# Kernel tuning notes

Measured on AMD Instinct MI355X. Metric: run time of the kernel, lower is better.

Reference implementation:

```python
import jax, jax.numpy as jnp
import numpy as np

BS, Q, S1, S2 = 8, 128, 32, 64
H_DIM, NH = 768, 12
DH = H_DIM // NH


def _linear_params(k, scale=0.02):
    kw, _ = jax.random.split(k)
    w = jax.random.normal(kw, (H_DIM, H_DIM), jnp.float32) * scale
    b = jnp.zeros((H_DIM,), jnp.float32)
    return w, b


def setup_inputs() -> dict:
    root = jax.random.key(0)
    ks = jax.random.split(root, 12)
    wq_w, wq_b = _linear_params(ks[0])
    wk_w, wk_b = _linear_params(ks[1])
    wv_w, wv_b = _linear_params(ks[2])
    sq_w, sq_b = _linear_params(ks[3])
    sk_w, sk_b = _linear_params(ks[4])
    sv_w, sv_b = _linear_params(ks[5])
    return {
        "q_in": jax.random.normal(ks[6], (BS, Q, H_DIM), jnp.float32),
        "k_in": jax.random.normal(ks[7], (BS, S1, S2, H_DIM), jnp.float32),
        "v_in": jax.random.normal(ks[8], (BS, S1, S2, H_DIM), jnp.float32),
        "kvec": jax.random.normal(ks[9], (BS, S1, H_DIM), jnp.float32),
        "word_mask": jnp.ones((BS, S1, S2), jnp.int32),
        "sentence_mask": jnp.ones((BS * Q, S1), jnp.int32),
        "wq_w": wq_w, "wq_b": wq_b, "wk_w": wk_w, "wk_b": wk_b,
        "wv_w": wv_w, "wv_b": wv_b, "sq_w": sq_w, "sq_b": sq_b,
        "sk_w": sk_w, "sk_b": sk_b, "sv_w": sv_w, "sv_b": sv_b,
    }


def reference(q_in, k_in, v_in, kvec, word_mask, sentence_mask,
              wq_w, wq_b, wk_w, wk_b, wv_w, wv_b,
              sq_w, sq_b, sk_w, sk_b, sv_w, sv_b):
    bs, q_len = q_in.shape[0], q_in.shape[1]
    s1, s2 = k_in.shape[1], k_in.shape[2]
    scale = 1.0 / jnp.sqrt(jnp.float32(DH))

    # additive masks, as in the torch module
    wm = (1.0 - word_mask.astype(jnp.float32)) * -10000.0      # [bs, s1, s2]
    sm = (1.0 - sentence_mask.astype(jnp.float32)) * -10000.0  # [bs*Q, s1]

    # ---- word-level attention ----
    q = (q_in @ wq_w + wq_b).reshape(bs, q_len, NH, DH)
    k = (k_in @ wk_w + wk_b).reshape(bs, s1, s2, NH, DH)
    v = (v_in @ wv_w + wv_b).reshape(bs, s1, s2, NH, DH)
    # scores over tokens within each sentence: [bs, s1, H, Q, s2]
    scores1 = jnp.einsum('bqhd,bsthd->bshqt', q, k) * scale
    probs1 = jax.nn.softmax(scores1 + wm[:, :, None, None, :], axis=-1)
    # word_hidden: [bs, Q, s1, h]
    wh = jnp.einsum('bshqt,bsthd->bqshd', probs1, v).reshape(bs, q_len, s1, H_DIM)

    # ---- sentence-level attention ----
    sq = (q_in @ sq_w + sq_b).reshape(bs, q_len, NH, DH)
    sk = (kvec @ sk_w + sk_b).reshape(bs, s1, NH, DH)   # shared across queries
    sv = (wh @ sv_w + sv_b).reshape(bs, q_len, s1, NH, DH)
    scores2 = jnp.einsum('bqhd,bshd->bqhs', sq, sk) * scale  # [bs, Q, H, s1]
    scores2 = scores2 + sm.reshape(bs, q_len, s1)[:, :, None, :]
    probs2 = jax.nn.softmax(scores2, axis=-1)
    out = jnp.einsum('bqhs,bqshd->bqhd', probs2, sv).reshape(bs * q_len, H_DIM)
    return out
```

## Files before the change

### kernel.cpp

```cpp
#include <hip/hip_runtime.h>
#include <hip/hip_bf16.h>


typedef __attribute__((ext_vector_type(8))) short short8;
typedef __attribute__((ext_vector_type(4))) short short4v;
typedef __attribute__((ext_vector_type(4))) float f32x4;

__device__ __forceinline__ short f2bf(float f) {
  __hip_bfloat16 b = __float2bfloat16(f);
  return __builtin_bit_cast(short, b);
}
__device__ __forceinline__ float bf2f(short s) {
  __hip_bfloat16 b = __builtin_bit_cast(__hip_bfloat16, s);
  return __bfloat162float(b);
}

#define MFMA16(a, b, c) __builtin_amdgcn_mfma_f32_16x16x32_bf16((a), (b), (c), 0, 0, 0)

__device__ __forceinline__ void async_load16(const void* g, void* l) {
  auto l3 = (__attribute__((address_space(3))) void*)(uintptr_t)(
      reinterpret_cast<uintptr_t>(l));
  auto g1 = (const __attribute__((address_space(1))) void*)g;
  __builtin_amdgcn_global_load_lds(g1, l3, 16, 0, 0);
}

__global__ __launch_bounds__(256)
void prep(const float* __restrict__ w0, const float* __restrict__ w1,
          const float* __restrict__ w2, const float* __restrict__ w3,
          const float* __restrict__ w4, const float* __restrict__ w5,
          short* __restrict__ WT,
          const float* __restrict__ q_in, const float* __restrict__ k_in,
          const float* __restrict__ v_in, const float* __restrict__ kvec,
          short* __restrict__ qbf, short* __restrict__ kbf,
          short* __restrict__ vbf, short* __restrict__ kvb) {
  const int id = blockIdx.x;
  const int tid = threadIdx.x;
  if (id < 3456) {
    __shared__ float tile[32][33];
    const int zz = id / 576, r = id % 576;
    const float* W = (zz == 0) ? w0 : (zz == 1) ? w1 : (zz == 2) ? w2
                   : (zz == 3) ? w3 : (zz == 4) ? w4 : w5;
    short* WTo = WT + (size_t)zz * 768 * 768;
    const int bx = (r % 24) * 32, by = (r / 24) * 32;
    const int tx = tid & 31, ty = tid >> 5;
    #pragma unroll
    for (int i = 0; i < 32; i += 8)
      tile[ty + i][tx] = W[(size_t)(by + ty + i) * 768 + bx + tx];
    __syncthreads();
    #pragma unroll
    for (int i = 0; i < 32; i += 8)
      WTo[(size_t)(bx + ty + i) * 768 + by + tx] = f2bf(tile[tx][ty + i]);
    return;
  }
  const int i = (id - 3456) * 256 + tid;
  const float* src;
  short* dst;
  int idx;
  if (i < 98304)        { src = q_in; dst = qbf; idx = i; }
  else if (i < 1671168) { src = k_in; dst = kbf; idx = i - 98304; }
  else if (i < 3244032) { src = v_in; dst = vbf; idx = i - 1671168; }
  else                  { src = kvec; dst = kvb; idx = i - 3244032; }
  const float4* s = (const float4*)src + (size_t)idx * 2;
  const float4 a = s[0], b = s[1];
  __align__(16) short tmp[8] = {f2bf(a.x), f2bf(a.y), f2bf(a.z), f2bf(a.w),
                                f2bf(b.x), f2bf(b.y), f2bf(b.z), f2bf(b.w)};
  *((short8*)dst + idx) = *(short8*)tmp;
}

__global__ __launch_bounds__(256)
void gemm_proj(const short* __restrict__ kbf, const short* __restrict__ vbf,
               const short* __restrict__ qbf, const short* __restrict__ kvb,
               const short* __restrict__ WT6,
               const float* __restrict__ wk_b, const float* __restrict__ wv_b,
               const float* __restrict__ wq_b, const float* __restrict__ sq_b,
               const float* __restrict__ sk_b,
               short* __restrict__ kp, short* __restrict__ vT,
               short* __restrict__ qp, float* __restrict__ sqp,
               float* __restrict__ skp) {
  const int K = 768, WELEM = 768 * 768;
  __shared__ __align__(16) short As[128 * 64];
  __shared__ __align__(16) short Bs[128 * 64];
  const int tid = threadIdx.x;
  const int w = tid >> 6, lane = tid & 63, quad = lane >> 4, l16 = lane & 15;
  const int wm = (w >> 1) * 64, wn = (w & 1) * 64;
  const f32x4 zero4 = {0.f, 0.f, 0.f, 0.f};

  if (blockIdx.z < 2) {
    const int z = blockIdx.z;
    const short* A = z ? vbf : kbf;
    const short* WT = z ? (WT6 + 3 * WELEM) : (WT6 + 2 * WELEM);
    const float* bias = z ? wv_b : wk_b;
    const int m0 = blockIdx.x * 128, n0 = blockIdx.y * 128;

    const int srow = lane >> 3;
    const int ssw = (lane & 7) ^ srow;
    const short* ag = A + (size_t)(m0 + w * 32 + srow) * K + ssw * 8;
    const short* bg = WT + (size_t)(n0 + w * 32 + srow) * K + ssw * 8;
    short* al = &As[(w * 32) * 64];
    short* bl = &Bs[(w * 32) * 64];
    const int fsw = l16 & 7;

    f32x4 acc[4][4];
    #pragma unroll
    for (int i = 0; i < 4; i++)
      #pragma unroll
      for (int j = 0; j < 4; j++) acc[i][j] = zero4;

    for (int k0 = 0; k0 < K; k0 += 64) {
      __syncthreads();
      #pragma unroll
      for (int ii = 0; ii < 4; ii++) {
        async_load16(ag + (size_t)ii * 8 * K, al + ii * 8 * 64);
        async_load16(bg + (size_t)ii * 8 * K, bl + ii * 8 * 64);
      }
      ag += 64;
      bg += 64;
      __syncthreads();
      #pragma unroll
      for (int kb2 = 0; kb2 < 2; kb2++) {
        short8 af[4], bf[4];
        #pragma unroll
        for (int i = 0; i < 4; i++)
          af[i] = *(short8*)&As[(wm + i * 16 + l16) * 64 +
                                (((kb2 * 4 + quad) ^ fsw) * 8)];
        #pragma unroll
        for (int j = 0; j < 4; j++)
          bf[j] = *(short8*)&Bs[(wn + j * 16 + l16) * 64 +
                                (((kb2 * 4 + quad) ^ fsw) * 8)];
        #pragma unroll
        for (int i = 0; i < 4; i++)
          #pragma unroll
          for (int j = 0; j < 4; j++)
            acc[i][j] = MFMA16(af[i], bf[j], acc[i][j]);
      }
    }

    if (z == 0) {
      #pragma unroll
      for (int i = 0; i < 4; i++)
        #pragma unroll
        for (int j = 0; j < 4; j++) {
          const int col = n0 + wn + j * 16 + l16;
          const float bv = bias[col];
          #pragma unroll
          for (int r = 0; r < 4; r++) {
            const int g = m0 + wm + i * 16 + quad * 4 + r;
            kp[(size_t)g * 768 + col] = f2bf(acc[i][j][r] + bv);
          }
        }
    } else {
      const int bs_ = (m0 + wm) >> 6;
      const int hh = (n0 + wn) >> 6;
      #pragma unroll
      for (int i = 0; i < 4; i++) {
        const int t0 = i * 16 + quad * 4;
        #pragma unroll
        for (int j = 0; j < 4; j++) {
          const int dd = j * 16 + l16;
          const float bv = bias[hh * 64 + dd];
          __align__(8) short tmp[4];
          #pragma unroll
          for (int r = 0; r < 4; r++) tmp[r] = f2bf(acc[i][j][r] + bv);
          *(short4v*)&vT[(((size_t)bs_ * 12 + hh) * 64 + dd) * 64 + t0] = *(short4v*)tmp;
        }
      }
    }
    return;
  }

  {
    const int id = blockIdx.x + 128 * blockIdx.y;
    if (id >= 108) return;
    const int qmode = (id < 96);
    const int r = qmode ? id : (id - 96);
    const int bx = qmode ? (r % 8) : (r % 2);
    const int by = qmode ? (r / 8) : (r / 2);
    const short* A = qmode ? qbf : kvb;
    const short* WT = qmode ? (WT6 + 0 * WELEM) : (WT6 + 4 * WELEM);

    const int m0 = bx * 128, n0 = by * 128;
    const int grow = w * 32 + (lane >> 2);
    const int kc = (lane & 3) * 8;
    const short* ag = A + (size_t)(m0 + grow) * K + kc;
    const short* bg = WT + (size_t)(n0 + grow) * K + kc;
    short* al = &As[(w * 32) * 32];
    short* bl = &Bs[(w * 32) * 32];

    f32x4 acc[4][4];
    #pragma unroll
    for (int i = 0; i < 4; i++)
      #pragma unroll
      for (int j = 0; j < 4; j++) acc[i][j] = zero4;

    for (int k0 = 0; k0 < K; k0 += 32) {
      __syncthreads();
      async_load16(ag, al);
      async_load16(ag + (size_t)16 * K, al + 16 * 32);
      async_load16(bg, bl);
      async_load16(bg + (size_t)16 * K, bl + 16 * 32);
      ag += 32;
      bg += 32;
      __syncthreads();
      short8 af[4], bf[4];
      #pragma unroll
      for (int i = 0; i < 4; i++)
        af[i] = *(short8*)&As[(wm + i * 16 + l16) * 32 + quad * 8];
      #pragma unroll
      for (int j = 0; j < 4; j++)
        bf[j] = *(short8*)&Bs[(wn + j * 16 + l16) * 32 + quad * 8];
      #pragma unroll
      for (int i = 0; i < 4; i++)
        #pragma unroll
        for (int j = 0; j < 4; j++)
          acc[i][j] = MFMA16(af[i], bf[j], acc[i][j]);
    }

    #pragma unroll
    for (int i = 0; i < 4; i++) {
      #pragma unroll
      for (int j = 0; j < 4; j++) {
        const int col = n0 + wn + j * 16 + l16;
        const float bv = qmode ? ((col < 768) ? wq_b[col] : sq_b[col - 768])
                               : sk_b[col];
        #pragma unroll
        for (int r4 = 0; r4 < 4; r4++) {
          const int g = m0 + wm + i * 16 + quad * 4 + r4;
          const float v = acc[i][j][r4] + bv;
          if (qmode) {
            if (col < 768) qp[(size_t)g * 768 + col] = f2bf(v * 0.125f);
            else sqp[(size_t)g * 768 + (col - 768)] = v;
          } else {
            skp[(size_t)g * 768 + col] = v;
          }
        }
      }
    }
  }
}

__global__ __launch_bounds__(256)
void wattn_sp(const short* __restrict__ q_proj, const short* __restrict__ k_proj,
              const short* __restrict__ vT, const int* __restrict__ word_mask,
              const float* __restrict__ sq, const float* __restrict__ sk,
              const int* __restrict__ sent_mask, short* __restrict__ wh,
              float* __restrict__ probs2) {
  __shared__ __align__(16) short KVs[128 * 72];
  __shared__ __align__(16) short Ps[128 * 72];
  const int bid = blockIdx.x;
  const int tid = threadIdx.x;

  if (bid >= 3072) {
    float* sc = (float*)KVs;
    const int bq = bid - 3072;
    const int b = bq >> 7, q = bq & 127;
    for (int p = tid; p < 384; p += 256) {
      const int hh = p >> 5, ss = p & 31;
      const float4* a = (const float4*)(sq + ((size_t)(b * 128 + q)) * 768 + hh * 64);
      const float4* c = (const float4*)(sk + ((size_t)(b * 32 + ss)) * 768 + hh * 64);
      float d = 0.f;
      #pragma unroll
      for (int i = 0; i < 16; i++) {
        const float4 av = a[i], cv = c[i];
        d += av.x * cv.x + av.y * cv.y + av.z * cv.z + av.w * cv.w;
      }
      d = d * 0.125f + (1.0f - (float)sent_mask[bq * 32 + ss]) * -10000.0f;
      sc[hh * 33 + ss] = d;
    }
    __syncthreads();
    if (tid < 12) {
      float mx = -3.0e38f;
      for (int ss = 0; ss < 32; ss++) mx = fmaxf(mx, sc[tid * 33 + ss]);
      float sum = 0.f;
      for (int ss = 0; ss < 32; ss++) {
        const float e = __expf(sc[tid * 33 + ss] - mx);
        sc[tid * 33 + ss] = e;
        sum += e;
      }
      const float inv = 1.0f / sum;
      for (int ss = 0; ss < 32; ss++) sc[tid * 33 + ss] *= inv;
    }
    __syncthreads();
    for (int p = tid; p < 384; p += 256) {
      const int hh = p >> 5, ss = p & 31;
      probs2[((size_t)bq * 12 + hh) * 32 + ss] = sc[hh * 33 + ss];
    }
    return;
  }

  short* Ks = KVs;
  short* Vs = KVs + 64 * 72;
  short* Os = KVs;
  const int h = bid % 12, s = (bid / 12) % 32, b = bid / (12 * 32);
  const int w = tid >> 6, lane = tid & 63, quad = lane >> 4, l16 = lane & 15;
  const f32x4 zero4 = {0.f, 0.f, 0.f, 0.f};

  {
    const int t2 = tid & 127;
    const int row8 = t2 >> 3;
    const int c8 = (t2 & 7) * 8;
    if (tid < 128) {
      const short* src = k_proj + ((size_t)((b * 32 + s) * 64)) * 768 + h * 64 + c8;
      #pragma unroll
      for (int i = 0; i < 4; i++) {
        const int r = row8 + i * 16;
        *(short8*)&Ks[r * 72 + c8] = *(const short8*)(src + (size_t)r * 768);
      }
    } else {
      const short* src = vT + ((size_t)((b * 32 + s) * 12 + h)) * 4096 + c8;
      #pragma unroll
      for (int i = 0; i < 4; i++) {
        const int r = row8 + i * 16;
        *(short8*)&Vs[r * 72 + c8] = *(const short8*)(src + (size_t)r * 64);
      }
    }
  }
  __syncthreads();

  f32x4 sac[2][4];
  #pragma unroll
  for (int i = 0; i < 2; i++)
    #pragma unroll
    for (int j = 0; j < 4; j++) sac[i][j] = zero4;
  {
    short8 aq[2][2], bk[4][2];
    #pragma unroll
    for (int i = 0; i < 2; i++)
      #pragma unroll
      for (int kb = 0; kb < 2; kb++)
        aq[i][kb] = *(const short8*)(q_proj +
            ((size_t)(b * 128 + w * 32 + i * 16 + l16)) * 768 + h * 64 + kb * 32 + quad * 8);
    #pragma unroll
    for (int j = 0; j < 4; j++)
      #pragma unroll
      for (int kb = 0; kb < 2; kb++)
        bk[j][kb] = *(short8*)&Ks[(j * 16 + l16) * 72 + kb * 32 + quad * 8];
    #pragma unroll
    for (int i = 0; i < 2; i++)
      #pragma unroll
      for (int j = 0; j < 4; j++) {
        sac[i][j] = MFMA16(aq[i][0], bk[j][0], sac[i][j]);
        sac[i][j] = MFMA16(aq[i][1], bk[j][1], sac[i][j]);
      }
  }

  {
    float wmv[4];
    const int* wmp = word_mask + (b * 32 + s) * 64;
    #pragma unroll
    for (int j = 0; j < 4; j++)
      wmv[j] = (1.0f - (float)wmp[j * 16 + l16]) * -10000.0f;
    #pragma unroll
    for (int i = 0; i < 2; i++) {
      #pragma unroll
      for (int r = 0; r < 4; r++) {
        float vv[4];
        float sum = 0.f;
        #pragma unroll
        for (int j = 0; j < 4; j++) {
          vv[j] = __expf(sac[i][j][r] + wmv[j]);
          sum += vv[j];
        }
        sum += __shfl_xor(sum, 1);
        sum += __shfl_xor(sum, 2);
        sum += __shfl_xor(sum, 4);
        sum += __shfl_xor(sum, 8);
        const float inv = 1.0f / sum;
        const int row = w * 32 + i * 16 + quad * 4 + r;
        #pragma unroll
        for (int j = 0; j < 4; j++)
          Ps[row * 72 + j * 16 + l16] = f2bf(vv[j] * inv);
      }
    }
  }
  __syncthreads();

  f32x4 oac[2][4];
  #pragma unroll
  for (int i = 0; i < 2; i++)
    #pragma unroll
    for (int j = 0; j < 4; j++) oac[i][j] = zero4;
  {
    short8 ap[2][2], bv[4][2];
    #pragma unroll
    for (int i = 0; i < 2; i++)
      #pragma unroll
      for (int kb = 0; kb < 2; kb++)
        ap[i][kb] = *(short8*)&Ps[(w * 32 + i * 16 + l16) * 72 + kb * 32 + quad * 8];
    #pragma unroll
    for (int j = 0; j < 4; j++)
      #pragma unroll
      for (int kb = 0; kb < 2; kb++)
        bv[j][kb] = *(short8*)&Vs[(j * 16 + l16) * 72 + kb * 32 + quad * 8];
    #pragma unroll
    for (int i = 0; i < 2; i++)
      #pragma unroll
      for (int j = 0; j < 4; j++) {
        oac[i][j] = MFMA16(ap[i][0], bv[j][0], oac[i][j]);
        oac[i][j] = MFMA16(ap[i][1], bv[j][1], oac[i][j]);
      }
  }
  __syncthreads();
  #pragma unroll
  for (int i = 0; i < 2; i++)
    #pragma unroll
    for (int j = 0; j < 4; j++)
      #pragma unroll
      for (int r = 0; r < 4; r++)
        Os[(w * 32 + i * 16 + quad * 4 + r) * 72 + j * 16 + l16] = f2bf(oac[i][j][r]);
  __syncthreads();

  {
    const int c8 = (tid & 7) * 8;
    #pragma unroll
    for (int i = 0; i < 4; i++) {
      const int row = i * 32 + (tid >> 3);
      short* dst = wh + (((size_t)(b * 128 + row)) * 32 + s) * 768 + h * 64;
      *(short8*)(dst + c8) = *(const short8*)&Os[row * 72 + c8];
    }
  }
}

__global__ __launch_bounds__(256)
void whc_kernel(const short* __restrict__ wh, const float* __restrict__ probs2,
                short* __restrict__ whc) {
  __shared__ __align__(16) short whs[32 * 776];
  __shared__ float p2s[384];
  const int bq = blockIdx.x, tid = threadIdx.x;
  const short8* src = (const short8*)(wh + (size_t)bq * 24576);
  for (int t = tid; t < 3072; t += 256) {
    const int row = t / 96, c8 = (t % 96) * 8;
    *(short8*)&whs[row * 776 + c8] = src[t];
  }
  for (int p = tid; p < 384; p += 256) p2s[p] = probs2[(size_t)bq * 384 + p];
  __syncthreads();

  float acc[3][12];
  #pragma unroll
  for (int kk = 0; kk < 3; kk++)
    #pragma unroll
    for (int h = 0; h < 12; h++) acc[kk][h] = 0.f;

  for (int s = 0; s < 32; s++) {
    float p2r[12];
    #pragma unroll
    for (int h = 0; h < 12; h++) p2r[h] = p2s[h * 32 + s];
    #pragma unroll
    for (int kk = 0; kk < 3; kk++) {
      const float wv = bf2f(whs[s * 776 + kk * 256 + tid]);
      #pragma unroll
      for (int h = 0; h < 12; h++) acc[kk][h] += p2r[h] * wv;
    }
  }
  #pragma unroll
  for (int h = 0; h < 12; h++)
    #pragma unroll
    for (int kk = 0; kk < 3; kk++)
      whc[((size_t)h * 1024 + bq) * 768 + kk * 256 + tid] = f2bf(acc[kk][h]);
}

__global__ __launch_bounds__(256)
void outg(const short* __restrict__ whc, const short* __restrict__ WTsv,
          const float* __restrict__ sv_b, float* __restrict__ out) {
  const int K = 768;
  __shared__ __align__(16) short As[128 * 32];
  __shared__ __align__(16) short Bs[64 * 32];
  const int tid = threadIdx.x;
  const int m0 = blockIdx.x * 128, h = blockIdx.y;
  const int w = tid >> 6, lane = tid & 63, quad = lane >> 4, l16 = lane & 15;
  const int wm = (w >> 1) * 64, wn = (w & 1) * 32;

  const int grow = w * 32 + (lane >> 2);
  const int kc = (lane & 3) * 8;
  const short* ag = whc + ((size_t)h * 1024 + m0 + grow) * K + kc;
  short* al = &As[(w * 32) * 32];
  const int growb = w * 16 + (lane >> 2);
  const short* bg = WTsv + (size_t)(h * 64 + growb) * K + kc;
  short* bl = &Bs[(w * 16) * 32];

  const f32x4 zero4 = {0.f, 0.f, 0.f, 0.f};
  f32x4 acc[4][2];
  #pragma unroll
  for (int i = 0; i < 4; i++)
    #pragma unroll
    for (int j = 0; j < 2; j++) acc[i][j] = zero4;

  for (int k0 = 0; k0 < K; k0 += 32) {
    __syncthreads();
    async_load16(ag, al);
    async_load16(ag + (size_t)16 * K, al + 16 * 32);
    async_load16(bg, bl);
    ag += 32;
    bg += 32;
    __syncthreads();
    short8 af[4], bf[2];
    #pragma unroll
    for (int i = 0; i < 4; i++)
      af[i] = *(short8*)&As[(wm + i * 16 + l16) * 32 + quad * 8];
    #pragma unroll
    for (int j = 0; j < 2; j++)
      bf[j] = *(short8*)&Bs[(wn + j * 16 + l16) * 32 + quad * 8];
    #pragma unroll
    for (int i = 0; i < 4; i++)
      #pragma unroll
      for (int j = 0; j < 2; j++)
        acc[i][j] = MFMA16(af[i], bf[j], acc[i][j]);
  }

  #pragma unroll
  for (int i = 0; i < 4; i++) {
    #pragma unroll
    for (int j = 0; j < 2; j++) {
      const int col = h * 64 + wn + j * 16 + l16;
      const float bv = sv_b[col];
      #pragma unroll
      for (int r = 0; r < 4; r++) {
        const int g = m0 + wm + i * 16 + quad * 4 + r;
        out[(size_t)g * 768 + col] = acc[i][j][r] + bv;
      }
    }
  }
}

extern "C" void kernel_launch(void* const* d_in, const int* in_sizes, int n_in,
                              void* d_out, int out_size, void* d_ws, size_t ws_size,
                              hipStream_t stream) {
  (void)in_sizes; (void)n_in; (void)out_size; (void)ws_size;
  const float* q_in      = (const float*)d_in[0];
  const float* k_in      = (const float*)d_in[1];
  const float* v_in      = (const float*)d_in[2];
  const float* kvec      = (const float*)d_in[3];
  const int*   word_mask = (const int*)d_in[4];
  const int*   sent_mask = (const int*)d_in[5];
  const float* wq_w = (const float*)d_in[6],  *wq_b = (const float*)d_in[7];
  const float* wk_w = (const float*)d_in[8],  *wk_b = (const float*)d_in[9];
  const float* wv_w = (const float*)d_in[10], *wv_b = (const float*)d_in[11];
  const float* sq_w = (const float*)d_in[12], *sq_b = (const float*)d_in[13];
  const float* sk_w = (const float*)d_in[14], *sk_b = (const float*)d_in[15];
  const float* sv_w = (const float*)d_in[16], *sv_b = (const float*)d_in[17];
  float* out = (float*)d_out;

  char* ws = (char*)d_ws;
  size_t off = 0;
  auto alloc = [&](size_t bytes) -> void* {
    void* p = ws + off;
    off += (bytes + 255) & ~(size_t)255;
    return p;
  };
  short* WT  = (short*)alloc((size_t)6 * 768 * 768 * 2);
  short* qbf = (short*)alloc((size_t)1024 * 768 * 2);
  short* kbf = (short*)alloc((size_t)16384 * 768 * 2);
  short* vbf = (short*)alloc((size_t)16384 * 768 * 2);
  short* kvb = (short*)alloc((size_t)256 * 768 * 2);
  short* qp  = (short*)alloc((size_t)1024 * 768 * 2);
  short* kp  = (short*)alloc((size_t)16384 * 768 * 2);
  short* vT  = (short*)alloc((size_t)16384 * 768 * 2);
  float* sqp = (float*)alloc((size_t)1024 * 768 * 4);
  float* skp = (float*)alloc((size_t)256 * 768 * 4);
  short* wh  = (short*)alloc((size_t)32768 * 768 * 2);
  float* pr2 = (float*)alloc((size_t)1024 * 12 * 32 * 4);
  short* whc = (short*)alloc((size_t)12 * 1024 * 768 * 2);

  const int WELEM = 768 * 768;

  prep<<<dim3(16224), 256, 0, stream>>>(wq_w, sq_w, wk_w, wv_w, sk_w, sv_w, WT,
                                        q_in, k_in, v_in, kvec, qbf, kbf, vbf, kvb);
  gemm_proj<<<dim3(128, 6, 3), 256, 0, stream>>>(
      kbf, vbf, qbf, kvb, WT, wk_b, wv_b, wq_b, sq_b, sk_b,
      kp, vT, qp, sqp, skp);
  wattn_sp<<<dim3(4096), 256, 0, stream>>>(qp, kp, vT, word_mask, sqp, skp,
                                           sent_mask, wh, pr2);
  whc_kernel<<<dim3(1024), 256, 0, stream>>>(wh, pr2, whc);
  outg<<<dim3(8, 12), 256, 0, stream>>>(whc, WT + 5 * WELEM, sv_b, out);
}
```

Measured before the change: 328.7 us.

## Retile K/V projection GEMM to 256x256 with 8 waves and double-buffered LDS pipeline

The K/V projection GEMM moves from 128x128 tiles with 4 waves and single-buffered LDS to 256x256 tiles with 8 waves (512 threads) and 128KB of dynamic shared memory. Global-to-LDS async loads are double-buffered and interleaved with the MFMA sub-blocks using explicit vmcnt waits, barriers and s_setprio, so memory latency overlaps compute and each staged byte is reused more. The small Q/sentence projection path is kept and runs only on the first 256 threads of the larger block. The cost is much higher register and LDS pressure per block, fewer blocks in the grid, and a hand-written schedule whose correctness depends on the exact waitcnt counts.

```diff
diff --git a/kernel.cpp b/kernel.cpp
--- a/kernel.cpp
+++ b/kernel.cpp
@@ -23,6 +23,14 @@
   auto g1 = (const __attribute__((address_space(1))) void*)g;
   __builtin_amdgcn_global_load_lds(g1, l3, 16, 0, 0);
 }
+
+#define KBAR()                                      \
+  do {                                              \
+    asm volatile("" ::: "memory");                  \
+    __builtin_amdgcn_s_barrier();                   \
+    asm volatile("" ::: "memory");                  \
+  } while (0)
+#define VMW(N) asm volatile("s_waitcnt vmcnt(" #N ")" ::: "memory")
 
 __global__ __launch_bounds__(256)
 void prep(const float* __restrict__ w0, const float* __restrict__ w1,
@@ -67,7 +75,7 @@
   *((short8*)dst + idx) = *(short8*)tmp;
 }
 
-__global__ __launch_bounds__(256)
+__global__ __launch_bounds__(512, 2)
 void gemm_proj(const short* __restrict__ kbf, const short* __restrict__ vbf,
                const short* __restrict__ qbf, const short* __restrict__ kvb,
                const short* __restrict__ WT6,
@@ -78,90 +86,120 @@
                short* __restrict__ qp, float* __restrict__ sqp,
                float* __restrict__ skp) {
   const int K = 768, WELEM = 768 * 768;
-  __shared__ __align__(16) short As[128 * 64];
-  __shared__ __align__(16) short Bs[128 * 64];
+  extern __shared__ __align__(16) char smem_c[];
+  short* smem = (short*)smem_c;
   const int tid = threadIdx.x;
   const int w = tid >> 6, lane = tid & 63, quad = lane >> 4, l16 = lane & 15;
-  const int wm = (w >> 1) * 64, wn = (w & 1) * 64;
   const f32x4 zero4 = {0.f, 0.f, 0.f, 0.f};
 
   if (blockIdx.z < 2) {
+    short* LA = smem;
+    short* LB = smem + 2 * 256 * 64;
     const int z = blockIdx.z;
-    const short* A = z ? vbf : kbf;
-    const short* WT = z ? (WT6 + 3 * WELEM) : (WT6 + 2 * WELEM);
+    const short* Ag = z ? vbf : kbf;
+    const short* Bg = z ? (WT6 + 3 * WELEM) : (WT6 + 2 * WELEM);
     const float* bias = z ? wv_b : wk_b;
-    const int m0 = blockIdx.x * 128, n0 = blockIdx.y * 128;
+    const int m0 = blockIdx.x * 256, n0 = blockIdx.y * 256;
+    const int wr = w >> 2, wc = w & 3;
 
     const int srow = lane >> 3;
-    const int ssw = (lane & 7) ^ srow;
-    const short* ag = A + (size_t)(m0 + w * 32 + srow) * K + ssw * 8;
-    const short* bg = WT + (size_t)(n0 + w * 32 + srow) * K + ssw * 8;
-    short* al = &As[(w * 32) * 64];
-    short* bl = &Bs[(w * 32) * 64];
+    const int schk = (lane & 7) ^ srow;
+    const short* ag0 = Ag + (size_t)(m0 + w * 8 + srow) * K + schk * 8;
+    const short* bg0 = Bg + (size_t)(n0 + w * 8 + srow) * K + schk * 8;
+    short* la0 = LA + (w * 8) * 64;
+    short* lb0 = LB + (w * 8) * 64;
     const int fsw = l16 & 7;
 
-    f32x4 acc[4][4];
-    #pragma unroll
-    for (int i = 0; i < 4; i++)
+    f32x4 acc[8][4];
+    #pragma unroll
+    for (int i = 0; i < 8; i++)
       #pragma unroll
       for (int j = 0; j < 4; j++) acc[i][j] = zero4;
 
-    for (int k0 = 0; k0 < K; k0 += 64) {
-      __syncthreads();
-      #pragma unroll
-      for (int ii = 0; ii < 4; ii++) {
-        async_load16(ag + (size_t)ii * 8 * K, al + ii * 8 * 64);
-        async_load16(bg + (size_t)ii * 8 * K, bl + ii * 8 * 64);
-      }
-      ag += 64;
-      bg += 64;
-      __syncthreads();
-      #pragma unroll
-      for (int kb2 = 0; kb2 < 2; kb2++) {
-        short8 af[4], bf[4];
-        #pragma unroll
-        for (int i = 0; i < 4; i++)
-          af[i] = *(short8*)&As[(wm + i * 16 + l16) * 64 +
-                                (((kb2 * 4 + quad) ^ fsw) * 8)];
-        #pragma unroll
-        for (int j = 0; j < 4; j++)
-          bf[j] = *(short8*)&Bs[(wn + j * 16 + l16) * 64 +
-                                (((kb2 * 4 + quad) ^ fsw) * 8)];
-        #pragma unroll
-        for (int i = 0; i < 4; i++)
-          #pragma unroll
-          for (int j = 0; j < 4; j++)
-            acc[i][j] = MFMA16(af[i], bf[j], acc[i][j]);
-      }
-    }
+    auto STG1 = [&](int op, int h, int kt) {
+      if (kt >= 12) kt -= 2;
+      const int buf = kt & 1;
+      const short* g = (op ? bg0 : ag0) + (size_t)h * 128 * K + (size_t)kt * 64;
+      short* lb = (op ? lb0 : la0) + buf * 16384 + h * (128 * 64);
+      async_load16(g, lb);
+      async_load16(g + (size_t)64 * K, lb + 64 * 64);
+    };
+
+    short8 af[4][2];
+    short8 bf2[2][2];
+
+#define LDA_(BUF, IH)                                                        \
+  _Pragma("unroll") for (int i = 0; i < 4; i++)                              \
+    _Pragma("unroll") for (int kb = 0; kb < 2; kb++)                         \
+      af[i][kb] = *(const short8*)&LA[(BUF)*16384 +                          \
+          (wr * 128 + (IH)*64 + i * 16 + l16) * 64 +                         \
+          (((kb * 4 + quad) ^ fsw) * 8)];
+#define LDB_(BUF, JH)                                                        \
+  _Pragma("unroll") for (int j = 0; j < 2; j++)                              \
+    _Pragma("unroll") for (int kb = 0; kb < 2; kb++)                         \
+      bf2[j][kb] = *(const short8*)&LB[(BUF)*16384 +                         \
+          (wc * 64 + (JH)*32 + j * 16 + l16) * 64 +                          \
+          (((kb * 4 + quad) ^ fsw) * 8)];
+#define MM_(IH, JH)                                                          \
+  __builtin_amdgcn_s_setprio(1);                                             \
+  _Pragma("unroll") for (int i = 0; i < 4; i++)                              \
+    _Pragma("unroll") for (int j = 0; j < 2; j++) {                          \
+      acc[(IH)*4 + i][(JH)*2 + j] =                                          \
+          MFMA16(af[i][0], bf2[j][0], acc[(IH)*4 + i][(JH)*2 + j]);          \
+      acc[(IH)*4 + i][(JH)*2 + j] =                                          \
+          MFMA16(af[i][1], bf2[j][1], acc[(IH)*4 + i][(JH)*2 + j]);          \
+    }                                                                        \
+  __builtin_amdgcn_s_setprio(0);
+
+    STG1(0, 0, 0); STG1(0, 1, 0); STG1(1, 0, 0); STG1(1, 1, 0);
+    STG1(0, 0, 1);
+    VMW(2);
+    KBAR();
+
+    #pragma unroll 1
+    for (int it = 0; it < 6; ++it) {
+      const int kb_t = 2 * it + 1, kc = 2 * it + 2, kd = 2 * it + 3;
+      LDA_(0, 0); LDB_(0, 0); STG1(0, 1, kb_t); KBAR(); MM_(0, 0); KBAR();
+      LDB_(0, 1); STG1(1, 0, kb_t); KBAR(); MM_(0, 1); KBAR();
+      LDA_(0, 1); LDB_(0, 0); STG1(1, 1, kb_t); KBAR(); MM_(1, 0); KBAR();
+      LDB_(0, 1); STG1(0, 0, kc); KBAR(); MM_(1, 1); VMW(2); KBAR();
+      LDA_(1, 0); LDB_(1, 0); STG1(0, 1, kc); KBAR(); MM_(0, 0); KBAR();
+      LDB_(1, 1); STG1(1, 0, kc); KBAR(); MM_(0, 1); KBAR();
+      LDA_(1, 1); LDB_(1, 0); STG1(1, 1, kc); KBAR(); MM_(1, 0); KBAR();
+      LDB_(1, 1); STG1(0, 0, kd); KBAR(); MM_(1, 1); VMW(2); KBAR();
+    }
+#undef LDA_
+#undef LDB_
+#undef MM_
 
     if (z == 0) {
       #pragma unroll
-      for (int i = 0; i < 4; i++)
-        #pragma unroll
-        for (int j = 0; j < 4; j++) {
-          const int col = n0 + wn + j * 16 + l16;
+      for (int I = 0; I < 8; I++)
+        #pragma unroll
+        for (int J = 0; J < 4; J++) {
+          const int col = n0 + wc * 64 + J * 16 + l16;
           const float bv = bias[col];
           #pragma unroll
           for (int r = 0; r < 4; r++) {
-            const int g = m0 + wm + i * 16 + quad * 4 + r;
-            kp[(size_t)g * 768 + col] = f2bf(acc[i][j][r] + bv);
+            const int g = m0 + wr * 128 + I * 16 + quad * 4 + r;
+            kp[(size_t)g * 768 + col] = f2bf(acc[I][J][r] + bv);
           }
         }
     } else {
-      const int bs_ = (m0 + wm) >> 6;
-      const int hh = (n0 + wn) >> 6;
-      #pragma unroll
-      for (int i = 0; i < 4; i++) {
-        const int t0 = i * 16 + quad * 4;
-        #pragma unroll
-        for (int j = 0; j < 4; j++) {
-          const int dd = j * 16 + l16;
+      const int hh = (n0 >> 6) + wc;
+      #pragma unroll
+      for (int I = 0; I < 8; I++) {
+        const int bs_ = (m0 >> 6) + wr * 2 + (I >> 2);
+        const int t0 = (I & 3) * 16 + quad * 4;
+        #pragma unroll
+        for (int J = 0; J < 4; J++) {
+          const int dd = J * 16 + l16;
           const float bv = bias[hh * 64 + dd];
           __align__(8) short tmp[4];
           #pragma unroll
-          for (int r = 0; r < 4; r++) tmp[r] = f2bf(acc[i][j][r] + bv);
-          *(short4v*)&vT[(((size_t)bs_ * 12 + hh) * 64 + dd) * 64 + t0] = *(short4v*)tmp;
+          for (int r = 0; r < 4; r++) tmp[r] = f2bf(acc[I][J][r] + bv);
+          *(short4v*)&vT[(((size_t)bs_ * 12 + hh) * 64 + dd) * 64 + t0] =
+              *(short4v*)tmp;
         }
       }
     }
@@ -169,8 +207,10 @@
   }
 
   {
-    const int id = blockIdx.x + 128 * blockIdx.y;
+    const int id = blockIdx.x + 64 * blockIdx.y;
     if (id >= 108) return;
+    short* As = smem;
+    short* Bs = smem + 128 * 32;
     const int qmode = (id < 96);
     const int r = qmode ? id : (id - 96);
     const int bx = qmode ? (r % 8) : (r % 2);
@@ -178,6 +218,7 @@
     const short* A = qmode ? qbf : kvb;
     const short* WT = qmode ? (WT6 + 0 * WELEM) : (WT6 + 4 * WELEM);
 
+    const int wm = (w >> 1) * 64, wn = (w & 1) * 64;
     const int m0 = bx * 128, n0 = by * 128;
     const int grow = w * 32 + (lane >> 2);
     const int kc = (lane & 3) * 8;
@@ -194,26 +235,31 @@
 
     for (int k0 = 0; k0 < K; k0 += 32) {
       __syncthreads();
-      async_load16(ag, al);
-      async_load16(ag + (size_t)16 * K, al + 16 * 32);
-      async_load16(bg, bl);
-      async_load16(bg + (size_t)16 * K, bl + 16 * 32);
+      if (tid < 256) {
+        async_load16(ag, al);
+        async_load16(ag + (size_t)16 * K, al + 16 * 32);
+        async_load16(bg, bl);
+        async_load16(bg + (size_t)16 * K, bl + 16 * 32);
+      }
       ag += 32;
       bg += 32;
       __syncthreads();
-      short8 af[4], bf[4];
-      #pragma unroll
-      for (int i = 0; i < 4; i++)
-        af[i] = *(short8*)&As[(wm + i * 16 + l16) * 32 + quad * 8];
-      #pragma unroll
-      for (int j = 0; j < 4; j++)
-        bf[j] = *(short8*)&Bs[(wn + j * 16 + l16) * 32 + quad * 8];
-      #pragma unroll
-      for (int i = 0; i < 4; i++)
+      if (tid < 256) {
+        short8 af[4], bf[4];
+        #pragma unroll
+        for (int i = 0; i < 4; i++)
+          af[i] = *(short8*)&As[(wm + i * 16 + l16) * 32 + quad * 8];
         #pragma unroll
         for (int j = 0; j < 4; j++)
-          acc[i][j] = MFMA16(af[i], bf[j], acc[i][j]);
-    }
+          bf[j] = *(short8*)&Bs[(wn + j * 16 + l16) * 32 + quad * 8];
+        #pragma unroll
+        for (int i = 0; i < 4; i++)
+          #pragma unroll
+          for (int j = 0; j < 4; j++)
+            acc[i][j] = MFMA16(af[i], bf[j], acc[i][j]);
+      }
+    }
+    if (tid >= 256) return;
 
     #pragma unroll
     for (int i = 0; i < 4; i++) {
@@ -538,6 +584,15 @@
   const float* sk_w = (const float*)d_in[14], *sk_b = (const float*)d_in[15];
   const float* sv_w = (const float*)d_in[16], *sv_b = (const float*)d_in[17];
   float* out = (float*)d_out;
+
+  const int WELEM = 768 * 768;
+
+  static bool s_attr_done = false;
+  if (!s_attr_done) {
+    (void)hipFuncSetAttribute(reinterpret_cast<const void*>(&gemm_proj),
+                              hipFuncAttributeMaxDynamicSharedMemorySize, 131072);
+    s_attr_done = true;
+  }
 
   char* ws = (char*)d_ws;
   size_t off = 0;
@@ -560,11 +615,9 @@
   float* pr2 = (float*)alloc((size_t)1024 * 12 * 32 * 4);
   short* whc = (short*)alloc((size_t)12 * 1024 * 768 * 2);
 
-  const int WELEM = 768 * 768;
-
   prep<<<dim3(16224), 256, 0, stream>>>(wq_w, sq_w, wk_w, wv_w, sk_w, sv_w, WT,
                                         q_in, k_in, v_in, kvec, qbf, kbf, vbf, kvb);
-  gemm_proj<<<dim3(128, 6, 3), 256, 0, stream>>>(
+  gemm_proj<<<dim3(64, 3, 3), 512, 131072, stream>>>(
       kbf, vbf, qbf, kvb, WT, wk_b, wv_b, wq_b, sq_b, sk_b,
       kp, vT, qp, sqp, skp);
   wattn_sp<<<dim3(4096), 256, 0, stream>>>(qp, kp, vT, word_mask, sqp, skp,
```

Measured after the change: 317.8 us. -3.3%, faster.
